# Optimization experiments

Measured on AMD Instinct MI355X. Metric: run time of the kernel, lower is better.

The kernel has to match this reference:

```python
import jax, jax.numpy as jnp
import numpy as np

VOCAB = 10000
EMBED = 100
T = 80
UNITS = 512
B = 4096
RATE = 0.2  # Keras LSTMCell dropout on inputs, 4 gate masks, cached across timesteps


def setup_inputs() -> dict:
    key = jax.random.key(0)
    ks = jax.random.split(key, 10)
    s = 0.05
    return {
        "inputs": jax.random.randint(ks[0], (B, T), 0, VOCAB, dtype=jnp.int32),
        "embed": jax.random.normal(ks[1], (VOCAB, EMBED), dtype=jnp.float32) * s,
        "W0": jax.random.normal(ks[2], (EMBED, 4 * UNITS), dtype=jnp.float32) * s,
        "U0": jax.random.normal(ks[3], (UNITS, 4 * UNITS), dtype=jnp.float32) * s,
        "b0": jnp.zeros((4 * UNITS,), dtype=jnp.float32),
        "W1": jax.random.normal(ks[4], (UNITS, 4 * UNITS), dtype=jnp.float32) * s,
        "U1": jax.random.normal(ks[5], (UNITS, 4 * UNITS), dtype=jnp.float32) * s,
        "b1": jnp.zeros((4 * UNITS,), dtype=jnp.float32),
        "Wout": jax.random.normal(ks[6], (UNITS, 1), dtype=jnp.float32) * s,
        "bout": jnp.zeros((1,), dtype=jnp.float32),
    }


def _dropout_masks(key, shape):
    keep = 1.0 - RATE
    return jax.random.bernoulli(key, keep, shape).astype(jnp.float32) / keep


def _lstm_cell(h, c, xt, masks, W, U, b, in_dim):
    # masks: [4, B, in_dim] per-gate input dropout masks (fixed across time)
    # kernel layout: W.reshape(in_dim, 4, UNITS), gate order i, f, g(cand), o
    z = jnp.einsum('gbd,dgh->bgh', xt[None] * masks, W.reshape(in_dim, 4, UNITS))
    z = z + (h @ U + b).reshape(-1, 4, UNITS)
    i = jax.nn.sigmoid(z[:, 0])
    f = jax.nn.sigmoid(z[:, 1])
    g = jnp.tanh(z[:, 2])
    o = jax.nn.sigmoid(z[:, 3])
    c_new = f * c + i * g
    h_new = o * jnp.tanh(c_new)
    return h_new, c_new


def reference(inputs, embed, W0, U0, b0, W1, U1, b1, Wout, bout):
    x = embed[inputs]                      # [B, T, EMBED]
    mkey = jax.random.key(42)
    k0, k1 = jax.random.split(mkey)
    m0 = _dropout_masks(k0, (4, B, EMBED))
    m1 = _dropout_masks(k1, (4, B, UNITS))

    def step(carry, xt):
        h0, c0, h1, c1 = carry
        h0, c0 = _lstm_cell(h0, c0, xt, m0, W0, U0, b0, EMBED)
        h1, c1 = _lstm_cell(h1, c1, h0, m1, W1, U1, b1, UNITS)
        return (h0, c0, h1, c1), None

    init = tuple(jnp.zeros((B, UNITS), dtype=jnp.float32) for _ in range(4))
    (h0, c0, h1, c1), _ = jax.lax.scan(step, init, jnp.swapaxes(x, 0, 1))
    return jax.nn.sigmoid(h1 @ Wout + bout)   # [B, 1]
```

## Files before the change

kernel.cpp:

```cpp
#include <hip/hip_runtime.h>
#include <hip/hip_bf16.h>
#include <stdint.h>

#define BATCH 4096
#define TT    80
#define EMB   100
#define UNITS 512
#define N4    2048
#define K0P   128

typedef unsigned short ushort;
typedef unsigned char uchar;
typedef __bf16 bf16x8 __attribute__((ext_vector_type(8)));
typedef float f32x4 __attribute__((ext_vector_type(4)));

__device__ __forceinline__ uint32_t rotl32(uint32_t x, uint32_t r) {
  return (x << r) | (x >> (32u - r));
}
__device__ __forceinline__ void tf_round4(uint32_t& x0, uint32_t& x1,
                                          int r0, int r1, int r2, int r3) {
  x0 += x1; x1 = rotl32(x1, r0); x1 ^= x0;
  x0 += x1; x1 = rotl32(x1, r1); x1 ^= x0;
  x0 += x1; x1 = rotl32(x1, r2); x1 ^= x0;
  x0 += x1; x1 = rotl32(x1, r3); x1 ^= x0;
}
__device__ __forceinline__ void tf2x32(uint32_t k0, uint32_t k1,
                                       uint32_t x0, uint32_t x1,
                                       uint32_t& y0, uint32_t& y1) {
  uint32_t k2 = k0 ^ k1 ^ 0x1BD11BDAu;
  x0 += k0; x1 += k1;
  tf_round4(x0, x1, 13, 15, 26, 6);  x0 += k1; x1 += k2 + 1u;
  tf_round4(x0, x1, 17, 29, 16, 24); x0 += k2; x1 += k0 + 2u;
  tf_round4(x0, x1, 13, 15, 26, 6);  x0 += k0; x1 += k1 + 3u;
  tf_round4(x0, x1, 17, 29, 16, 24); x0 += k1; x1 += k2 + 4u;
  tf_round4(x0, x1, 13, 15, 26, 6);  x0 += k2; x1 += k0 + 5u;
  y0 = x0; y1 = x1;
}
__device__ __forceinline__ int keepbit(uint32_t u) {
  float f = __uint_as_float((u >> 9) | 0x3F800000u) - 1.0f;
  return f < 0.8f ? 1 : 0;
}

__device__ __forceinline__ ushort f2bf(float f) {
  uint32_t u = __float_as_uint(f);
  uint32_t r = (u + 0x7FFFu + ((u >> 16) & 1u)) >> 16;
  return (ushort)r;
}
__device__ __forceinline__ float bf2f(ushort u) {
  return __uint_as_float(((uint32_t)u) << 16);
}

#define M0N (4 * BATCH * EMB)
#define M1N (4 * BATCH * UNITS)

__global__ __launch_bounds__(256) void masks_kernel(uchar* __restrict__ m0p,
                                                    uchar* __restrict__ m1p) {
  uint32_t k0a, k0b, k1a, k1b;
  tf2x32(0u, 42u, 0u, 0u, k0a, k0b);
  tf2x32(0u, 42u, 0u, 1u, k1a, k1b);
  const int n0 = BATCH * EMB;
  const int n1 = BATCH * UNITS;
  const int total = n0 + n1;
  for (int i = blockIdx.x * blockDim.x + threadIdx.x; i < total;
       i += gridDim.x * blockDim.x) {
    if (i < n0) {
      uchar byte = 0;
#pragma unroll
      for (int g = 0; g < 4; g++) {
        uint32_t y0, y1;
        tf2x32(k0a, k0b, 0u, (uint32_t)(g * n0 + i), y0, y1);
        byte |= keepbit(y0 ^ y1) << g;
      }
      m0p[i] = byte;
    } else {
      int j = i - n0;
      uchar byte = 0;
#pragma unroll
      for (int g = 0; g < 4; g++) {
        uint32_t y0, y1;
        tf2x32(k1a, k1b, 0u, (uint32_t)(g * n1 + j), y0, y1);
        byte |= keepbit(y0 ^ y1) << g;
      }
      m1p[j] = byte;
    }
  }
}

__global__ __launch_bounds__(256) void convT(const float* __restrict__ src,
                                             ushort* __restrict__ dst,
                                             int Ksrc, int Kpad) {
  __shared__ float t[32][33];
  const int n0 = blockIdx.x * 32, kk0 = blockIdx.y * 32;
  const int tx = threadIdx.x & 31, ty = threadIdx.x >> 5;
#pragma unroll
  for (int r = ty; r < 32; r += 8) {
    const int k = kk0 + r;
    t[r][tx] = (k < Ksrc) ? src[(size_t)k * N4 + n0 + tx] : 0.f;
  }
  __syncthreads();
#pragma unroll
  for (int r = ty; r < 32; r += 8)
    dst[(size_t)(n0 + r) * Kpad + kk0 + tx] = f2bf(t[tx][r]);
}

__device__ __forceinline__ void xm0_prep_one(int i, int t,
                                             const int* __restrict__ inputs,
                                             const float* __restrict__ embed,
                                             const uchar* __restrict__ m0p,
                                             ushort* __restrict__ Xm0) {
  const int k = i & 127;
  const int b = (i >> 7) & 4095;
  const int g = i >> 19;
  float v = 0.f;
  if (k < EMB) {
    const int idx = inputs[b * TT + t];
    const float e = embed[(size_t)idx * EMB + k];
    v = ((m0p[b * EMB + k] >> g) & 1) ? e * 1.25f : 0.f;
  }
  Xm0[((size_t)g << 19) + (b << 7) + k] = f2bf(v);
}

__global__ __launch_bounds__(256) void prep0_kernel(const int* __restrict__ inputs,
                                                    const float* __restrict__ embed,
                                                    const uchar* __restrict__ m0p,
                                                    ushort* __restrict__ Xm0) {
  const int i = blockIdx.x * blockDim.x + threadIdx.x;
  xm0_prep_one(i, 0, inputs, embed, m0p, Xm0);
}

__device__ __forceinline__ void gload16(const void* g, void* l) {
  __builtin_amdgcn_global_load_lds(
      (const __attribute__((address_space(1))) unsigned int*)g,
      (__attribute__((address_space(3))) unsigned int*)l, 16, 0, 0);
}

__global__ __launch_bounds__(256) void cell_gemm_mfma(
    const ushort* __restrict__ A1, int K1,
    const ushort* __restrict__ B1,
    const ushort* __restrict__ A2,
    const ushort* __restrict__ B2,
    const float* __restrict__ bias,
    float* __restrict__ z) {
  __shared__ __align__(16) ushort As[128 * 32];
  __shared__ __align__(16) ushort Bs[128 * 32];

  const int tid = threadIdx.x;
  const int w = tid >> 6, l = tid & 63;
  const int bm0 = blockIdx.x * 128, bn0 = blockIdx.y * 128;
  const int gate = bn0 >> 9;
  const int wm = (w >> 1) * 64, wn = (w & 1) * 64;
  const int fr = l & 15, kq = l >> 4;
  const int schunk = (l & 3) * 8;
  const int srow_l = l >> 2;

  f32x4 acc[4][4] = {};

  const ushort* A1g = A1 + (size_t)gate * BATCH * K1;

#pragma unroll 1
  for (int seg = 0; seg < 2; seg++) {
    const ushort* A = seg ? A2 : A1g;
    const ushort* B = seg ? B2 : B1;
    const int K = seg ? UNITS : K1;
#pragma unroll 1
    for (int k0 = 0; k0 < K; k0 += 32) {
#pragma unroll
      for (int c2 = 0; c2 < 2; c2++) {
        const int r = (w * 2 + c2) * 16 + srow_l;
        gload16(A + (size_t)(bm0 + r) * K + k0 + schunk,
                (void*)(As + (w * 2 + c2) * 512));
        gload16(B + (size_t)(bn0 + r) * K + k0 + schunk,
                (void*)(Bs + (w * 2 + c2) * 512));
      }
      __syncthreads();
      bf16x8 a[4], b[4];
#pragma unroll
      for (int f = 0; f < 4; f++) {
        a[f] = *(const bf16x8*)&As[(wm + f * 16 + fr) * 32 + kq * 8];
        b[f] = *(const bf16x8*)&Bs[(wn + f * 16 + fr) * 32 + kq * 8];
      }
#pragma unroll
      for (int fi = 0; fi < 4; fi++)
#pragma unroll
        for (int fj = 0; fj < 4; fj++)
          acc[fi][fj] = __builtin_amdgcn_mfma_f32_16x16x32_bf16(
              a[fi], b[fj], acc[fi][fj], 0, 0, 0);
      __syncthreads();
    }
  }

#pragma unroll
  for (int fi = 0; fi < 4; fi++) {
#pragma unroll
    for (int fj = 0; fj < 4; fj++) {
      const int n = bn0 + wn + fj * 16 + fr;
      const float bv = bias[n];
#pragma unroll
      for (int j = 0; j < 4; j++) {
        const int m = bm0 + wm + fi * 16 + kq * 4 + j;
        z[(size_t)m * N4 + n] = acc[fi][fj][j] + bv;
      }
    }
  }
}

__global__ __launch_bounds__(256) void gates0_kernel(
    const float* __restrict__ z, float* __restrict__ c0,
    ushort* __restrict__ h0b, ushort* __restrict__ H0m,
    const uchar* __restrict__ m1p) {
  const int i = blockIdx.x * blockDim.x + threadIdx.x;
  const int b = i >> 9, h = i & 511;
  const float* zb = z + (size_t)b * N4;
  const float zi = zb[h], zf = zb[512 + h], zg = zb[1024 + h], zo = zb[1536 + h];
  const float iv = 1.f / (1.f + __expf(-zi));
  const float fv = 1.f / (1.f + __expf(-zf));
  const float gv = tanhf(zg);
  const float ov = 1.f / (1.f + __expf(-zo));
  const float cn = fv * c0[i] + iv * gv;
  c0[i] = cn;
  const float hn = ov * tanhf(cn);
  h0b[i] = f2bf(hn);
  const uchar mb = m1p[i];
  const float hm = hn * 1.25f;
#pragma unroll
  for (int g = 0; g < 4; g++)
    H0m[(size_t)g * (BATCH * UNITS) + i] = f2bf((mb >> g) & 1 ? hm : 0.f);
}

__global__ __launch_bounds__(256) void gates1_kernel(
    const float* __restrict__ z, float* __restrict__ c1,
    ushort* __restrict__ h1b,
    const int* __restrict__ inputs, const float* __restrict__ embed,
    const uchar* __restrict__ m0p, ushort* __restrict__ Xm0, int tnext) {
  const int i = blockIdx.x * blockDim.x + threadIdx.x;
  const int b = i >> 9, h = i & 511;
  const float* zb = z + (size_t)b * N4;
  const float zi = zb[h], zf = zb[512 + h], zg = zb[1024 + h], zo = zb[1536 + h];
  const float iv = 1.f / (1.f + __expf(-zi));
  const float fv = 1.f / (1.f + __expf(-zf));
  const float gv = tanhf(zg);
  const float ov = 1.f / (1.f + __expf(-zo));
  const float cn = fv * c1[i] + iv * gv;
  c1[i] = cn;
  h1b[i] = f2bf(ov * tanhf(cn));
  if (tnext < TT) xm0_prep_one(i, tnext, inputs, embed, m0p, Xm0);
}

__global__ __launch_bounds__(256) void out_kernel(const ushort* __restrict__ h1b,
                                                  const float* __restrict__ Wout,
                                                  const float* __restrict__ bout,
                                                  float* __restrict__ out) {
  const int wid = (blockIdx.x * blockDim.x + threadIdx.x) >> 6;
  const int lane = threadIdx.x & 63;
  if (wid >= BATCH) return;
  const ushort* hr = h1b + (size_t)wid * UNITS;
  float s = 0.f;
#pragma unroll
  for (int j = 0; j < UNITS; j += 64) s += bf2f(hr[j + lane]) * Wout[j + lane];
  for (int off = 32; off; off >>= 1) s += __shfl_down(s, off, 64);
  if (lane == 0) out[wid] = 1.f / (1.f + __expf(-(s + bout[0])));
}

extern "C" void kernel_launch(void* const* d_in, const int* in_sizes, int n_in,
                              void* d_out, int out_size, void* d_ws, size_t ws_size,
                              hipStream_t stream) {
  const int* inputs = (const int*)d_in[0];
  const float* embed = (const float*)d_in[1];
  const float* W0 = (const float*)d_in[2];
  const float* U0 = (const float*)d_in[3];
  const float* b0 = (const float*)d_in[4];
  const float* W1 = (const float*)d_in[5];
  const float* U1 = (const float*)d_in[6];
  const float* b1 = (const float*)d_in[7];
  const float* Wout = (const float*)d_in[8];
  const float* bout = (const float*)d_in[9];
  float* out = (float*)d_out;

  char* ws = (char*)d_ws;
  float* z    = (float*)(ws + 0);
  float* c0   = (float*)(ws + 33554432);
  float* c1   = (float*)(ws + 41943040);
  ushort* h0b = (ushort*)(ws + 50331648);
  ushort* h1b = (ushort*)(ws + 54525952);
  ushort* H0m = (ushort*)(ws + 58720256);
  ushort* Xm0 = (ushort*)(ws + 75497472);
  ushort* W0T = (ushort*)(ws + 79691776);
  ushort* U0T = (ushort*)(ws + 80216064);
  ushort* W1T = (ushort*)(ws + 82313216);
  ushort* U1T = (ushort*)(ws + 84410368);
  uchar* m0p  = (uchar*)(ws + 86507520);
  uchar* m1p  = (uchar*)(ws + 86917120);

  hipMemsetAsync(ws + 33554432, 0, 25165824, stream);

  masks_kernel<<<2048, 256, 0, stream>>>(m0p, m1p);

  {
    dim3 g0(N4 / 32, K0P / 32);
    convT<<<g0, 256, 0, stream>>>(W0, W0T, EMB, K0P);
    dim3 g1(N4 / 32, UNITS / 32);
    convT<<<g1, 256, 0, stream>>>(U0, U0T, UNITS, UNITS);
    convT<<<g1, 256, 0, stream>>>(W1, W1T, UNITS, UNITS);
    convT<<<g1, 256, 0, stream>>>(U1, U1T, UNITS, UNITS);
  }

  prep0_kernel<<<(4 * BATCH * K0P) / 256, 256, 0, stream>>>(inputs, embed, m0p, Xm0);

  const dim3 grid(BATCH / 128, N4 / 128);
  const int gblocks = (BATCH * UNITS) / 256;
  for (int t = 0; t < TT; t++) {
    cell_gemm_mfma<<<grid, 256, 0, stream>>>(Xm0, K0P, W0T, h0b, U0T, b0, z);
    gates0_kernel<<<gblocks, 256, 0, stream>>>(z, c0, h0b, H0m, m1p);
    cell_gemm_mfma<<<grid, 256, 0, stream>>>(H0m, UNITS, W1T, h1b, U1T, b1, z);
    gates1_kernel<<<gblocks, 256, 0, stream>>>(z, c1, h1b, inputs, embed, m0p,
                                               Xm0, t + 1);
  }

  out_kernel<<<BATCH * 64 / 256, 256, 0, stream>>>(h1b, Wout, bout, out);
}
```

Measured before the change: 6.032 ms.

## Fuse gate GEMMs with activations and wavefront-pipeline both LSTM layers per launch

Replaces the separate GEMM and gate kernels with one fused kernel. Each block computes all four gates for a 128x64 tile and applies the LSTM activations in registers, so the fp32 z buffer no longer makes a round trip through memory. Layer 1 at step k, layer 0 at step k+1 and the embedding prep for step k+2 now run in a single launch, with ping-pong buffers for h, H0m and Xm0. This cuts four launches per step to one and overlaps the two layers. The cost is more registers per block (a 2x2x8 accumulator array) and more complex buffer indexing.

New measurement: 11.39 ms. +88.9%, slower.

```diff
diff --git a/kernel.cpp b/kernel.cpp
--- a/kernel.cpp
+++ b/kernel.cpp
@@ -40,7 +40,6 @@
   float f = __uint_as_float((u >> 9) | 0x3F800000u) - 1.0f;
   return f < 0.8f ? 1 : 0;
 }
-
 __device__ __forceinline__ ushort f2bf(float f) {
   uint32_t u = __float_as_uint(f);
   uint32_t r = (u + 0x7FFFu + ((u >> 16) & 1u)) >> 16;
@@ -49,9 +48,6 @@
 __device__ __forceinline__ float bf2f(ushort u) {
   return __uint_as_float(((uint32_t)u) << 16);
 }
-
-#define M0N (4 * BATCH * EMB)
-#define M1N (4 * BATCH * UNITS)
 
 __global__ __launch_bounds__(256) void masks_kernel(uchar* __restrict__ m0p,
                                                     uchar* __restrict__ m1p) {
@@ -120,12 +116,14 @@
   Xm0[((size_t)g << 19) + (b << 7) + k] = f2bf(v);
 }
 
-__global__ __launch_bounds__(256) void prep0_kernel(const int* __restrict__ inputs,
-                                                    const float* __restrict__ embed,
-                                                    const uchar* __restrict__ m0p,
-                                                    ushort* __restrict__ Xm0) {
+__global__ __launch_bounds__(256) void prep_x2(const int* __restrict__ inputs,
+                                               const float* __restrict__ embed,
+                                               const uchar* __restrict__ m0p,
+                                               ushort* __restrict__ Xm0_0,
+                                               ushort* __restrict__ Xm0_1) {
   const int i = blockIdx.x * blockDim.x + threadIdx.x;
-  xm0_prep_one(i, 0, inputs, embed, m0p, Xm0);
+  if (i < (1 << 21)) xm0_prep_one(i, 0, inputs, embed, m0p, Xm0_0);
+  else xm0_prep_one(i - (1 << 21), 1, inputs, embed, m0p, Xm0_1);
 }
 
 __device__ __forceinline__ void gload16(const void* g, void* l) {
@@ -134,116 +132,173 @@
       (__attribute__((address_space(3))) unsigned int*)l, 16, 0, 0);
 }
 
-__global__ __launch_bounds__(256) void cell_gemm_mfma(
-    const ushort* __restrict__ A1, int K1,
-    const ushort* __restrict__ B1,
-    const ushort* __restrict__ A2,
-    const ushort* __restrict__ B2,
+__device__ __forceinline__ void cell_part(
+    int bid, int tid,
+    const ushort* __restrict__ Am, size_t gstride, int Km,
+    const ushort* __restrict__ Ash,
+    const ushort* __restrict__ WT,
+    const ushort* __restrict__ UT,
     const float* __restrict__ bias,
-    float* __restrict__ z) {
-  __shared__ __align__(16) ushort As[128 * 32];
-  __shared__ __align__(16) ushort Bs[128 * 32];
-
-  const int tid = threadIdx.x;
+    float* __restrict__ c,
+    ushort* __restrict__ h_wr,
+    ushort* __restrict__ H0m_wr,
+    const uchar* __restrict__ m1p,
+    ushort* smem) {
   const int w = tid >> 6, l = tid & 63;
-  const int bm0 = blockIdx.x * 128, bn0 = blockIdx.y * 128;
-  const int gate = bn0 >> 9;
-  const int wm = (w >> 1) * 64, wn = (w & 1) * 64;
   const int fr = l & 15, kq = l >> 4;
+  const int srow = l >> 2;
   const int schunk = (l & 3) * 8;
-  const int srow_l = l >> 2;
-
-  f32x4 acc[4][4] = {};
-
-  const ushort* A1g = A1 + (size_t)gate * BATCH * K1;
-
-#pragma unroll 1
-  for (int seg = 0; seg < 2; seg++) {
-    const ushort* A = seg ? A2 : A1g;
-    const ushort* B = seg ? B2 : B1;
-    const int K = seg ? UNITS : K1;
-#pragma unroll 1
-    for (int k0 = 0; k0 < K; k0 += 32) {
+  const int cid = (bid & 7) * 32 + (bid >> 3);
+  const int bm0 = (cid >> 3) * 128;
+  const int bh0 = (cid & 7) * 64;
+  ushort* Bs = smem + 16384;
+
+  f32x4 acc[2][2][8] = {};
+
+  for (int k0 = 0; k0 < Km; k0 += 32) {
+#pragma unroll
+    for (int g = 0; g < 4; g++)
 #pragma unroll
       for (int c2 = 0; c2 < 2; c2++) {
-        const int r = (w * 2 + c2) * 16 + srow_l;
-        gload16(A + (size_t)(bm0 + r) * K + k0 + schunk,
-                (void*)(As + (w * 2 + c2) * 512));
-        gload16(B + (size_t)(bn0 + r) * K + k0 + schunk,
-                (void*)(Bs + (w * 2 + c2) * 512));
-      }
-      __syncthreads();
-      bf16x8 a[4], b[4];
-#pragma unroll
-      for (int f = 0; f < 4; f++) {
-        a[f] = *(const bf16x8*)&As[(wm + f * 16 + fr) * 32 + kq * 8];
-        b[f] = *(const bf16x8*)&Bs[(wn + f * 16 + fr) * 32 + kq * 8];
-      }
-#pragma unroll
-      for (int fi = 0; fi < 4; fi++)
-#pragma unroll
-        for (int fj = 0; fj < 4; fj++)
-          acc[fi][fj] = __builtin_amdgcn_mfma_f32_16x16x32_bf16(
-              a[fi], b[fj], acc[fi][fj], 0, 0, 0);
-      __syncthreads();
+        const int row = w * 32 + c2 * 16;
+        gload16(Am + (size_t)g * gstride + (size_t)(bm0 + row + srow) * Km +
+                    k0 + schunk,
+                smem + (g * 128 + row) * 32);
+      }
+#pragma unroll
+    for (int s = 0; s < 2; s++)
+#pragma unroll
+      for (int c2 = 0; c2 < 2; c2++) {
+        const int jb = w * 32 + c2 * 16;
+        const int j = jb + srow;
+        gload16(WT + (size_t)((j >> 5) * 512 + bh0 + s * 32 + (j & 31)) * Km +
+                    k0 + schunk,
+                Bs + s * 4096 + jb * 32);
+      }
+    __syncthreads();
+    bf16x8 bfr[2][8], am[4][2];
+#pragma unroll
+    for (int s = 0; s < 2; s++)
+#pragma unroll
+      for (int fj = 0; fj < 8; fj++)
+        bfr[s][fj] = *(const bf16x8*)&Bs[s * 4096 + (fj * 16 + fr) * 32 + kq * 8];
+#pragma unroll
+    for (int g = 0; g < 4; g++)
+#pragma unroll
+      for (int fi = 0; fi < 2; fi++)
+        am[g][fi] =
+            *(const bf16x8*)&smem[(g * 128 + w * 32 + fi * 16 + fr) * 32 + kq * 8];
+#pragma unroll
+    for (int s = 0; s < 2; s++)
+#pragma unroll
+      for (int fi = 0; fi < 2; fi++)
+#pragma unroll
+        for (int fj = 0; fj < 8; fj++)
+          acc[s][fi][fj] = __builtin_amdgcn_mfma_f32_16x16x32_bf16(
+              am[fj >> 1][fi], bfr[s][fj], acc[s][fi][fj], 0, 0, 0);
+    __syncthreads();
+  }
+
+  for (int k0 = 0; k0 < 512; k0 += 32) {
+#pragma unroll
+    for (int c2 = 0; c2 < 2; c2++) {
+      const int row = w * 32 + c2 * 16;
+      gload16(Ash + (size_t)(bm0 + row + srow) * 512 + k0 + schunk,
+              smem + row * 32);
     }
-  }
-
-#pragma unroll
-  for (int fi = 0; fi < 4; fi++) {
-#pragma unroll
-    for (int fj = 0; fj < 4; fj++) {
-      const int n = bn0 + wn + fj * 16 + fr;
-      const float bv = bias[n];
-#pragma unroll
-      for (int j = 0; j < 4; j++) {
-        const int m = bm0 + wm + fi * 16 + kq * 4 + j;
-        z[(size_t)m * N4 + n] = acc[fi][fj][j] + bv;
+#pragma unroll
+    for (int s = 0; s < 2; s++)
+#pragma unroll
+      for (int c2 = 0; c2 < 2; c2++) {
+        const int jb = w * 32 + c2 * 16;
+        const int j = jb + srow;
+        gload16(UT + (size_t)((j >> 5) * 512 + bh0 + s * 32 + (j & 31)) * 512 +
+                    k0 + schunk,
+                Bs + s * 4096 + jb * 32);
+      }
+    __syncthreads();
+    bf16x8 bfr[2][8], a2[2];
+#pragma unroll
+    for (int s = 0; s < 2; s++)
+#pragma unroll
+      for (int fj = 0; fj < 8; fj++)
+        bfr[s][fj] = *(const bf16x8*)&Bs[s * 4096 + (fj * 16 + fr) * 32 + kq * 8];
+#pragma unroll
+    for (int fi = 0; fi < 2; fi++)
+      a2[fi] = *(const bf16x8*)&smem[(w * 32 + fi * 16 + fr) * 32 + kq * 8];
+#pragma unroll
+    for (int s = 0; s < 2; s++)
+#pragma unroll
+      for (int fi = 0; fi < 2; fi++)
+#pragma unroll
+        for (int fj = 0; fj < 8; fj++)
+          acc[s][fi][fj] = __builtin_amdgcn_mfma_f32_16x16x32_bf16(
+              a2[fi], bfr[s][fj], acc[s][fi][fj], 0, 0, 0);
+    __syncthreads();
+  }
+
+#pragma unroll
+  for (int s = 0; s < 2; s++) {
+#pragma unroll
+    for (int hf = 0; hf < 2; hf++) {
+      const int h = bh0 + s * 32 + hf * 16 + fr;
+      const float bvi = bias[h];
+      const float bvf = bias[512 + h];
+      const float bvg = bias[1024 + h];
+      const float bvo = bias[1536 + h];
+#pragma unroll
+      for (int fi = 0; fi < 2; fi++) {
+#pragma unroll
+        for (int jj = 0; jj < 4; jj++) {
+          const int r = bm0 + w * 32 + fi * 16 + kq * 4 + jj;
+          const float zi = acc[s][fi][0 + hf][jj] + bvi;
+          const float zf = acc[s][fi][2 + hf][jj] + bvf;
+          const float zg = acc[s][fi][4 + hf][jj] + bvg;
+          const float zo = acc[s][fi][6 + hf][jj] + bvo;
+          const float iv = 1.f / (1.f + __expf(-zi));
+          const float fv = 1.f / (1.f + __expf(-zf));
+          const float gv = tanhf(zg);
+          const float ov = 1.f / (1.f + __expf(-zo));
+          const size_t ci = (size_t)r * 512 + h;
+          const float cn = fv * c[ci] + iv * gv;
+          c[ci] = cn;
+          const float hn = ov * tanhf(cn);
+          h_wr[ci] = f2bf(hn);
+          if (H0m_wr) {
+            const uchar mb = m1p[ci];
+            const float hm = hn * 1.25f;
+#pragma unroll
+            for (int g = 0; g < 4; g++)
+              H0m_wr[((size_t)g << 21) + ci] = f2bf((mb >> g) & 1 ? hm : 0.f);
+          }
+        }
       }
     }
   }
 }
 
-__global__ __launch_bounds__(256) void gates0_kernel(
-    const float* __restrict__ z, float* __restrict__ c0,
-    ushort* __restrict__ h0b, ushort* __restrict__ H0m,
-    const uchar* __restrict__ m1p) {
-  const int i = blockIdx.x * blockDim.x + threadIdx.x;
-  const int b = i >> 9, h = i & 511;
-  const float* zb = z + (size_t)b * N4;
-  const float zi = zb[h], zf = zb[512 + h], zg = zb[1024 + h], zo = zb[1536 + h];
-  const float iv = 1.f / (1.f + __expf(-zi));
-  const float fv = 1.f / (1.f + __expf(-zf));
-  const float gv = tanhf(zg);
-  const float ov = 1.f / (1.f + __expf(-zo));
-  const float cn = fv * c0[i] + iv * gv;
-  c0[i] = cn;
-  const float hn = ov * tanhf(cn);
-  h0b[i] = f2bf(hn);
-  const uchar mb = m1p[i];
-  const float hm = hn * 1.25f;
-#pragma unroll
-  for (int g = 0; g < 4; g++)
-    H0m[(size_t)g * (BATCH * UNITS) + i] = f2bf((mb >> g) & 1 ? hm : 0.f);
-}
-
-__global__ __launch_bounds__(256) void gates1_kernel(
-    const float* __restrict__ z, float* __restrict__ c1,
-    ushort* __restrict__ h1b,
-    const int* __restrict__ inputs, const float* __restrict__ embed,
-    const uchar* __restrict__ m0p, ushort* __restrict__ Xm0, int tnext) {
-  const int i = blockIdx.x * blockDim.x + threadIdx.x;
-  const int b = i >> 9, h = i & 511;
-  const float* zb = z + (size_t)b * N4;
-  const float zi = zb[h], zf = zb[512 + h], zg = zb[1024 + h], zo = zb[1536 + h];
-  const float iv = 1.f / (1.f + __expf(-zi));
-  const float fv = 1.f / (1.f + __expf(-zf));
-  const float gv = tanhf(zg);
-  const float ov = 1.f / (1.f + __expf(-zo));
-  const float cn = fv * c1[i] + iv * gv;
-  c1[i] = cn;
-  h1b[i] = f2bf(ov * tanhf(cn));
-  if (tnext < TT) xm0_prep_one(i, tnext, inputs, embed, m0p, Xm0);
+__global__ __launch_bounds__(256) void fused_step(
+    int t, int nl1, int nl0, int naux,
+    const ushort* H0m_rd, const ushort* h1_rd, ushort* h1_wr, float* c1,
+    const ushort* W1T, const ushort* U1T, const float* b1,
+    const ushort* Xm0_rd, const ushort* h0_rd, ushort* h0_wr, ushort* H0m_wr,
+    float* c0, const ushort* W0T, const ushort* U0T, const float* b0,
+    const uchar* m1p,
+    const int* inputs, const float* embed, const uchar* m0p, ushort* Xm0_wr) {
+  __shared__ __align__(16) ushort smem[24576];
+  const int bid = blockIdx.x, tid = threadIdx.x;
+  if (bid < nl1) {
+    cell_part(bid, tid, H0m_rd, (size_t)1 << 21, 512, h1_rd, W1T, U1T, b1, c1,
+              h1_wr, nullptr, nullptr, smem);
+  } else if (bid < nl1 + nl0) {
+    cell_part(bid - nl1, tid, Xm0_rd, (size_t)1 << 19, K0P, h0_rd, W0T, U0T, b0,
+              c0, h0_wr, H0m_wr, m1p, smem);
+  } else {
+    const int i0 = (bid - nl1 - nl0) * 256 + tid;
+    const int stride = naux * 256;
+    for (int i = i0; i < (1 << 21); i += stride)
+      xm0_prep_one(i, t + 2, inputs, embed, m0p, Xm0_wr);
+  }
 }
 
 __global__ __launch_bounds__(256) void out_kernel(const ushort* __restrict__ h1b,
@@ -277,24 +332,31 @@
   float* out = (float*)d_out;
 
   char* ws = (char*)d_ws;
-  float* z    = (float*)(ws + 0);
-  float* c0   = (float*)(ws + 33554432);
-  float* c1   = (float*)(ws + 41943040);
-  ushort* h0b = (ushort*)(ws + 50331648);
-  ushort* h1b = (ushort*)(ws + 54525952);
-  ushort* H0m = (ushort*)(ws + 58720256);
-  ushort* Xm0 = (ushort*)(ws + 75497472);
-  ushort* W0T = (ushort*)(ws + 79691776);
-  ushort* U0T = (ushort*)(ws + 80216064);
-  ushort* W1T = (ushort*)(ws + 82313216);
-  ushort* U1T = (ushort*)(ws + 84410368);
-  uchar* m0p  = (uchar*)(ws + 86507520);
-  uchar* m1p  = (uchar*)(ws + 86917120);
-
-  hipMemsetAsync(ws + 33554432, 0, 25165824, stream);
+  float* c0     = (float*)(ws + 0);
+  float* c1     = (float*)(ws + 8388608);
+  ushort* h0b1  = (ushort*)(ws + 16777216);
+  ushort* h1b1  = (ushort*)(ws + 20971520);
+  ushort* h0b0  = (ushort*)(ws + 25165824);
+  ushort* h1b0  = (ushort*)(ws + 29360128);
+  ushort* H0m0  = (ushort*)(ws + 33554432);
+  ushort* H0m1  = (ushort*)(ws + 50331648);
+  ushort* Xm00  = (ushort*)(ws + 67108864);
+  ushort* Xm01  = (ushort*)(ws + 71303168);
+  ushort* W0T   = (ushort*)(ws + 75497472);
+  ushort* U0T   = (ushort*)(ws + 76021760);
+  ushort* W1T   = (ushort*)(ws + 78118912);
+  ushort* U1T   = (ushort*)(ws + 80216064);
+  uchar* m0p    = (uchar*)(ws + 82313216);
+  uchar* m1p    = (uchar*)(ws + 82722816);
+
+  ushort* h0b[2] = {h0b0, h0b1};
+  ushort* h1b[2] = {h1b0, h1b1};
+  ushort* H0m[2] = {H0m0, H0m1};
+  ushort* Xm0[2] = {Xm00, Xm01};
+
+  hipMemsetAsync(ws, 0, 25165824, stream);
 
   masks_kernel<<<2048, 256, 0, stream>>>(m0p, m1p);
-
   {
     dim3 g0(N4 / 32, K0P / 32);
     convT<<<g0, 256, 0, stream>>>(W0, W0T, EMB, K0P);
@@ -303,18 +365,22 @@
     convT<<<g1, 256, 0, stream>>>(W1, W1T, UNITS, UNITS);
     convT<<<g1, 256, 0, stream>>>(U1, U1T, UNITS, UNITS);
   }
-
-  prep0_kernel<<<(4 * BATCH * K0P) / 256, 256, 0, stream>>>(inputs, embed, m0p, Xm0);
-
-  const dim3 grid(BATCH / 128, N4 / 128);
-  const int gblocks = (BATCH * UNITS) / 256;
-  for (int t = 0; t < TT; t++) {
-    cell_gemm_mfma<<<grid, 256, 0, stream>>>(Xm0, K0P, W0T, h0b, U0T, b0, z);
-    gates0_kernel<<<gblocks, 256, 0, stream>>>(z, c0, h0b, H0m, m1p);
-    cell_gemm_mfma<<<grid, 256, 0, stream>>>(H0m, UNITS, W1T, h1b, U1T, b1, z);
-    gates1_kernel<<<gblocks, 256, 0, stream>>>(z, c1, h1b, inputs, embed, m0p,
-                                               Xm0, t + 1);
-  }
-
-  out_kernel<<<BATCH * 64 / 256, 256, 0, stream>>>(h1b, Wout, bout, out);
-}
+  prep_x2<<<(2 << 21) / 256, 256, 0, stream>>>(inputs, embed, m0p, Xm00, Xm01);
+
+  fused_step<<<256, 256, 0, stream>>>(
+      -1, 0, 256, 0, H0m0, h1b1, h1b0, c1, W1T, U1T, b1, Xm00, h0b1, h0b0,
+      H0m0, c0, W0T, U0T, b0, m1p, inputs, embed, m0p, Xm00);
+
+  for (int k = 0; k < TT; k++) {
+    const int pt = k & 1, pn = pt ^ 1;
+    const int nl0 = (k < TT - 1) ? 256 : 0;
+    const int naux = (k < TT - 2) ? 64 : 0;
+    fused_step<<<256 + nl0 + naux, 256, 0, stream>>>(
+        k, 256, nl0, naux,
+        H0m[pt], h1b[pn], h1b[pt], c1, W1T, U1T, b1,
+        Xm0[pn], h0b[pt], h0b[pn], H0m[pn], c0, W0T, U0T, b0, m1p,
+        inputs, embed, m0p, Xm0[pt]);
+  }
+
+  out_kernel<<<BATCH * 64 / 256, 256, 0, stream>>>(h1b[1], Wout, bout, out);
+}
```
